# Kernel tuning notes

Measured on AMD Instinct MI355X. Metric: run time of the kernel, lower is better.

Reference implementation:

```python
import jax, jax.numpy as jnp
import numpy as np

B, CIN, COUT, H, W = 8, 128, 256, 64, 64
EPS = 1e-5


def conv2d(x, w, b, pad):
    y = jax.lax.conv_general_dilated(
        x, w, window_strides=(1, 1), padding=[(pad, pad), (pad, pad)],
        dimension_numbers=('NCHW', 'OIHW', 'NCHW'))
    return y + b[None, :, None, None]


def deform_sample(x, offset):
    # x: [B,C,H,W], offset: [B,18,H,W] -> sampled: [B,C,9,H,W]
    b, c, h, w = x.shape
    off = offset.reshape(b, 9, 2, h, w)  # (dy, dx) per kernel tap (torchvision v1 order)
    ky = (jnp.arange(9) // 3 - 1).astype(x.dtype)
    kx = (jnp.arange(9) % 3 - 1).astype(x.dtype)
    py = jnp.arange(h, dtype=x.dtype)[None, None, :, None] + ky[None, :, None, None] + off[:, :, 0]
    px = jnp.arange(w, dtype=x.dtype)[None, None, None, :] + kx[None, :, None, None] + off[:, :, 1]
    y0 = jnp.floor(py); x0 = jnp.floor(px)
    fy = py - y0;       fx = px - x0
    xf = x.reshape(b, c, h * w)

    def gather(iy, ix):
        valid = (iy >= 0) & (iy < h) & (ix >= 0) & (ix < w)
        iyc = jnp.clip(iy, 0, h - 1).astype(jnp.int32)
        ixc = jnp.clip(ix, 0, w - 1).astype(jnp.int32)
        idx = (iyc * w + ixc).reshape(b, -1)  # [B, 9*H*W]
        g = jax.vmap(lambda xb, ib: jnp.take(xb, ib, axis=1))(xf, idx)  # [B,C,9HW]
        return g.reshape(b, c, 9, h, w) * valid.astype(x.dtype)[:, None]

    samp = (gather(y0,     x0    ) * ((1 - fy) * (1 - fx))[:, None]
          + gather(y0,     x0 + 1) * ((1 - fy) * fx      )[:, None]
          + gather(y0 + 1, x0    ) * (fy * (1 - fx)      )[:, None]
          + gather(y0 + 1, x0 + 1) * (fy * fx            )[:, None])
    return samp


def setup_inputs():
    key = jax.random.key(0)
    ks = jax.random.split(key, 8)
    return {
        'x':     jax.random.normal(ks[0], (B, CIN, H, W), jnp.float32),
        'w_off': jax.random.normal(ks[1], (18, CIN, 3, 3), jnp.float32) * 0.01,
        'b_off': jnp.zeros((18,), jnp.float32),
        'w_def': jax.random.normal(ks[2], (COUT, CIN, 3, 3), jnp.float32) * 0.03,
        'b_def': jax.random.normal(ks[3], (COUT,), jnp.float32) * 0.01,
        'gamma': jnp.ones((COUT,), jnp.float32),
        'beta':  jnp.zeros((COUT,), jnp.float32),
        'w_sc':  jax.random.normal(ks[4], (COUT, CIN, 1, 1), jnp.float32) * 0.05,
        'b_sc':  jnp.zeros((COUT,), jnp.float32),
    }


def reference(x, w_off, b_off, w_def, b_def, gamma, beta, w_sc, b_sc):
    offset = conv2d(x, w_off, b_off, pad=1)                 # [B,18,H,W]
    samp = deform_sample(x, offset)                         # [B,C,9,H,W]
    out = jnp.einsum('bckhw,ock->bohw', samp, w_def.reshape(COUT, CIN, 9))
    out = out + b_def[None, :, None, None]
    # BatchNorm2d (training mode: batch statistics)
    mean = out.mean(axis=(0, 2, 3))
    var = out.var(axis=(0, 2, 3))
    out = (out - mean[None, :, None, None]) * jax.lax.rsqrt(var + EPS)[None, :, None, None]
    out = out * gamma[None, :, None, None] + beta[None, :, None, None]
    out = out + conv2d(x, w_sc, b_sc, pad=0)                # residual shortcut (1x1)
    return jax.nn.relu(out)
```

## Files before the change

### kernel.cpp

```cpp
#include <hip/hip_runtime.h>

typedef __attribute__((ext_vector_type(8))) short bf16x8;
typedef __attribute__((ext_vector_type(4))) float f32x4;

__device__ __forceinline__ float bf2f(unsigned short u) {
  return __uint_as_float(((unsigned int)u) << 16);
}
__device__ __forceinline__ unsigned short f2bf(float f) {
  unsigned int u = __float_as_uint(f);
  u += 0x7fffu + ((u >> 16) & 1u);
  return (unsigned short)(u >> 16);
}

constexpr size_t OFF_XPAD = 0;
constexpr size_t SZ_XPAD  = (size_t)8 * 66 * 66 * 128 * 2;
constexpr size_t OFF_WB   = OFF_XPAD + SZ_XPAD;
constexpr size_t SZ_WB    = (size_t)9 * 16 * 256 * 8 * 2;
constexpr size_t OFF_WS2  = OFF_WB + SZ_WB;
constexpr size_t SZ_WS2   = (size_t)16 * 256 * 8 * 2;
constexpr size_t OFF_WO   = OFF_WS2 + SZ_WS2;
constexpr size_t SZ_WO    = (size_t)9 * 16 * 32 * 8 * 2;
constexpr size_t OFF_YM   = OFF_WO + SZ_WO;
constexpr size_t SZ_YM    = (size_t)32768 * 256 * 2;
constexpr size_t OFF_PART = OFF_YM + SZ_YM;
constexpr size_t SZ_PART  = (size_t)1024 * 256 * 2 * 4;
constexpr size_t OFF_STAT = OFF_PART + SZ_PART;

__global__ __launch_bounds__(256) void k_prep_x(const float* __restrict__ x,
                                                unsigned short* __restrict__ xp) {
  int blk = blockIdx.x;
  int b = blk >> 6, h = blk & 63;
  int t = threadIdx.x;
  __shared__ float tile[16][66];

  {
    unsigned short* base = xp + (size_t)b * 66 * 66 * 128;
    ushort4 z4 = {0, 0, 0, 0};
    if (t < 64) {
      int col = (t >> 5) ? 65 : 0;
      int i = t & 31;
      *(ushort4*)(base + ((size_t)(h + 1) * 66 + col) * 128 + i * 4) = z4;
    }
    if (h == 0) {
      for (int i = t; i < 2112; i += 256) {
        *(ushort4*)(base + (size_t)i * 4) = z4;
        *(ushort4*)(base + (size_t)65 * 66 * 128 + (size_t)i * 4) = z4;
      }
    }
  }

  for (int cc = 0; cc < 8; ++cc) {
    int c0 = cc * 16;
    int wr = t & 63, cl = t >> 6;
#pragma unroll
    for (int i = 0; i < 4; ++i) {
      int c = c0 + cl * 4 + i;
      tile[cl * 4 + i][wr] = x[(((size_t)b * 128 + c) * 64 + h) * 64 + wr];
    }
    __syncthreads();
    int ww = t >> 2, cq = t & 3;
    ushort4 u4;
    u4.x = f2bf(tile[cq * 4 + 0][ww]);
    u4.y = f2bf(tile[cq * 4 + 1][ww]);
    u4.z = f2bf(tile[cq * 4 + 2][ww]);
    u4.w = f2bf(tile[cq * 4 + 3][ww]);
    *(ushort4*)(xp + ((size_t)(b * 66 + h + 1) * 66 + (ww + 1)) * 128 + c0 + cq * 4) = u4;
    __syncthreads();
  }
}

__global__ __launch_bounds__(256) void k_pack_w(const float* __restrict__ wdef,
                                                const float* __restrict__ wsc,
                                                const float* __restrict__ woff,
                                                unsigned short* __restrict__ wB,
                                                unsigned short* __restrict__ wS,
                                                unsigned short* __restrict__ wO) {
  int tid = blockIdx.x * 256 + threadIdx.x;
  if (tid < 294912) {
    int k8 = tid & 7, n = (tid >> 3) & 255, kb = (tid >> 11) & 15, tap = tid >> 15;
    int c = kb * 8 + k8;
    wB[tid] = f2bf(wdef[((size_t)n * 128 + c) * 9 + tap]);
  } else if (tid < 294912 + 32768) {
    int i = tid - 294912;
    int k8 = i & 7, n = (i >> 3) & 255, kb = i >> 11;
    wS[i] = f2bf(wsc[(size_t)n * 128 + kb * 8 + k8]);
  } else if (tid < 294912 + 32768 + 36864) {
    int i = tid - 327680;
    int k8 = i & 7, n = (i >> 3) & 31, kb = (i >> 8) & 15, tap = i >> 12;
    int c = kb * 8 + k8;
    wO[i] = f2bf(n < 18 ? woff[((size_t)n * 128 + c) * 9 + tap] : 0.f);
  }
}

__global__ __launch_bounds__(256) void k_main(const unsigned short* __restrict__ xp,
                                              const unsigned short* __restrict__ wB,
                                              const unsigned short* __restrict__ wO,
                                              const float* __restrict__ boff,
                                              const float* __restrict__ bdef,
                                              unsigned short* __restrict__ ymain,
                                              float* __restrict__ partials) {
  int blk = blockIdx.x;
  int b = blk >> 7, rem = blk & 127, h = rem >> 1, half = rem & 1;
  int px0 = half * 32;
  int t = threadIdx.x;
  int lane = t & 63, wid = t >> 6;
  int m = lane & 15, quad = lane >> 4;
  __shared__ __align__(16) unsigned short At[2][32 * 136];
  __shared__ float offsL[9][32][2];

  if (wid < 2) {
    f32x4 a0 = {0.f, 0.f, 0.f, 0.f}, a1 = {0.f, 0.f, 0.f, 0.f};
    int px = px0 + wid * 16 + m;
    const unsigned short* xbase = xp + ((size_t)(b * 66 + h) * 66 + px) * 128 + quad * 8;
    for (int tap = 0; tap < 9; ++tap) {
      const unsigned short* arow = xbase + ((tap / 3) * 66 + (tap % 3)) * 128;
#pragma unroll
      for (int kk = 0; kk < 4; ++kk) {
        bf16x8 a = *(const bf16x8*)(arow + kk * 32);
        const unsigned short* bb = wO + (size_t)(tap * 16 + kk * 4 + quad) * 256;
        bf16x8 b0 = *(const bf16x8*)(bb + m * 8);
        bf16x8 b1 = *(const bf16x8*)(bb + (16 + m) * 8);
        a0 = __builtin_amdgcn_mfma_f32_16x16x32_bf16(a, b0, a0, 0, 0, 0);
        a1 = __builtin_amdgcn_mfma_f32_16x16x32_bf16(a, b1, a1, 0, 0, 0);
      }
    }
#pragma unroll
    for (int r = 0; r < 4; ++r) {
      int pxs = wid * 16 + quad * 4 + r;
      offsL[m >> 1][pxs][m & 1] = a0[r] + boff[m];
      if (m < 2) offsL[8][pxs][m] = a1[r] + boff[16 + m];
    }
  }
  __syncthreads();

  f32x4 acc[2][4];
#pragma unroll
  for (int i = 0; i < 2; ++i)
#pragma unroll
    for (int j = 0; j < 4; ++j) acc[i][j] = (f32x4){0.f, 0.f, 0.f, 0.f};

  int px_s = t >> 3, sub = t & 7;
  const unsigned short* xb_base = xp + (size_t)b * 66 * 66 * 128;
  int nb = wid * 64;

  auto sample_prep = [&](int tap, float* wgt, const unsigned short** p) {
    float2 ov = *(const float2*)&offsL[tap][px_s][0];
    int ky = tap / 3 - 1, kx = tap % 3 - 1;
    float py = (float)(h + ky) + ov.x;
    float pxf = (float)(px0 + px_s + kx) + ov.y;
    float y0f = floorf(py), x0f = floorf(pxf);
    float fy = py - y0f, fx = pxf - x0f;
    int iy0 = (int)y0f, ix0 = (int)x0f;
#pragma unroll
    for (int j = 0; j < 4; ++j) {
      int iy = iy0 + (j >> 1), ix = ix0 + (j & 1);
      float wy = (j >> 1) ? fy : 1.f - fy;
      float wx = (j & 1) ? fx : 1.f - fx;
      bool valid = (iy >= 0) && (iy < 64) && (ix >= 0) && (ix < 64);
      int iyc = min(max(iy, 0), 63), ixc = min(max(ix, 0), 63);
      wgt[j] = valid ? wy * wx : 0.f;
      p[j] = xb_base + ((size_t)(iyc + 1) * 66 + (ixc + 1)) * 128 + sub * 8;
    }
  };
  auto load_g1 = [&](const unsigned short** p, int g, bf16x8* v) {
#pragma unroll
    for (int j = 0; j < 4; ++j)
      v[j] = *(const bf16x8*)(p[j] + g * 64);
  };
  auto store_g1 = [&](unsigned short* dst, int g, const float* wgt, bf16x8* v) {
    bf16x8 o;
#pragma unroll
    for (int j = 0; j < 8; ++j) {
      float s = fmaf(wgt[0], bf2f((unsigned short)v[0][j]),
                fmaf(wgt[1], bf2f((unsigned short)v[1][j]),
                fmaf(wgt[2], bf2f((unsigned short)v[2][j]),
                     wgt[3] * bf2f((unsigned short)v[3][j]))));
      o[j] = (short)f2bf(s);
    }
    *(bf16x8*)(dst + g * 64) = o;
  };
  auto mfma_half = [&](const unsigned short* buf, int tap, int kk0) {
#pragma unroll
    for (int kk = kk0; kk < kk0 + 2; ++kk) {
      bf16x8 af[2];
#pragma unroll
      for (int ms = 0; ms < 2; ++ms)
        af[ms] = *(const bf16x8*)(buf + (ms * 16 + m) * 136 + kk * 32 + quad * 8);
#pragma unroll
      for (int ns = 0; ns < 4; ++ns) {
        bf16x8 bfr = *(const bf16x8*)(wB + ((size_t)(tap * 16 + kk * 4 + quad) * 256 + nb + ns * 16 + m) * 8);
#pragma unroll
        for (int ms = 0; ms < 2; ++ms)
          acc[ms][ns] = __builtin_amdgcn_mfma_f32_16x16x32_bf16(af[ms], bfr, acc[ms][ns], 0, 0, 0);
      }
    }
  };

  {
    float wgt[4]; const unsigned short* p[4]; bf16x8 v0[4], v1[4];
    sample_prep(0, wgt, p);
    unsigned short* dst = &At[0][px_s * 136 + sub * 8];
    load_g1(p, 0, v0); load_g1(p, 1, v1);
    store_g1(dst, 0, wgt, v0); store_g1(dst, 1, wgt, v1);
  }
#pragma unroll
  for (int tap = 0; tap < 9; ++tap) {
    __syncthreads();
    const unsigned short* cur = At[tap & 1];
    unsigned short* dst = &At[(tap + 1) & 1][px_s * 136 + sub * 8];
    if (tap < 8) {
      float wgt[4]; const unsigned short* p[4]; bf16x8 v0[4], v1[4];
      sample_prep(tap + 1, wgt, p);
      load_g1(p, 0, v0);
      load_g1(p, 1, v1);
      mfma_half(cur, tap, 0);
      store_g1(dst, 0, wgt, v0);
      mfma_half(cur, tap, 2);
      store_g1(dst, 1, wgt, v1);
    } else {
      mfma_half(cur, tap, 0);
      mfma_half(cur, tap, 2);
    }
  }

  __syncthreads();
  unsigned short* yb = &At[0][0];
#pragma unroll
  for (int ns = 0; ns < 4; ++ns) {
    int n = nb + ns * 16 + m;
    float bias = bdef[n];
    float s = 0.f, q = 0.f;
#pragma unroll
    for (int ms = 0; ms < 2; ++ms) {
#pragma unroll
      for (int r = 0; r < 4; ++r) {
        int px = ms * 16 + quad * 4 + r;
        float v = acc[ms][ns][r] + bias;
        yb[px * 264 + n] = f2bf(v);
        s += v;
        q += v * v;
      }
    }
    s += __shfl_xor(s, 16); s += __shfl_xor(s, 32);
    q += __shfl_xor(q, 16); q += __shfl_xor(q, 32);
    if (quad == 0) {
      partials[((size_t)blk * 256 + n) * 2 + 0] = s;
      partials[((size_t)blk * 256 + n) * 2 + 1] = q;
    }
  }
  __syncthreads();
  {
    unsigned short* grow = ymain + (size_t)(blk * 32 + px_s) * 256;
    const unsigned short* lrow = yb + px_s * 264;
#pragma unroll
    for (int k = 0; k < 4; ++k) {
      int n0 = k * 64 + sub * 8;
      *(bf16x8*)(grow + n0) = *(const bf16x8*)(lrow + n0);
    }
  }
}

__global__ __launch_bounds__(64) void k_stats(const float* __restrict__ partials,
                                              const float* __restrict__ gamma,
                                              const float* __restrict__ beta,
                                              float* __restrict__ stats) {
  int ch = blockIdx.x;
  int L = threadIdx.x;
  float s = 0.f, q = 0.f;
#pragma unroll
  for (int i = 0; i < 16; ++i) {
    int row = i * 64 + L;
    float2 pq = *(const float2*)&partials[((size_t)row * 256 + ch) * 2];
    s += pq.x;
    q += pq.y;
  }
#pragma unroll
  for (int d = 1; d < 64; d <<= 1) { s += __shfl_xor(s, d); q += __shfl_xor(q, d); }
  if (L == 0) {
    float mean = s * (1.f / 32768.f);
    float var = q * (1.f / 32768.f) - mean * mean;
    float inv = rsqrtf(var + 1e-5f);
    float A = gamma[ch] * inv;
    stats[ch * 2 + 0] = A;
    stats[ch * 2 + 1] = beta[ch] - mean * A;
  }
}

__global__ __launch_bounds__(256) void k_final(const unsigned short* __restrict__ xp,
                                               const unsigned short* __restrict__ wS,
                                               const unsigned short* __restrict__ ymain,
                                               const float* __restrict__ stats,
                                               const float* __restrict__ bsc,
                                               float* __restrict__ out) {
  int blk = blockIdx.x;
  int b = blk >> 7, rem = blk & 127, h = rem >> 1, half = rem & 1;
  int px0 = half * 32;
  int t = threadIdx.x;
  int lane = t & 63, wid = t >> 6;
  int m = lane & 15, quad = lane >> 4;
  __shared__ float tr[128 * 35];
  f32x4 acc[2][4];
#pragma unroll
  for (int i = 0; i < 2; ++i)
#pragma unroll
    for (int j = 0; j < 4; ++j) acc[i][j] = (f32x4){0.f, 0.f, 0.f, 0.f};
  const unsigned short* xrow = xp + ((size_t)(b * 66 + h + 1) * 66 + 1 + px0) * 128;
  int nb = wid * 64;
#pragma unroll
  for (int kk = 0; kk < 4; ++kk) {
    bf16x8 af[2];
#pragma unroll
    for (int ms = 0; ms < 2; ++ms)
      af[ms] = *(const bf16x8*)(xrow + (ms * 16 + m) * 128 + kk * 32 + quad * 8);
#pragma unroll
    for (int ns = 0; ns < 4; ++ns) {
      bf16x8 bfr = *(const bf16x8*)(wS + ((size_t)(kk * 4 + quad) * 256 + nb + ns * 16 + m) * 8);
#pragma unroll
      for (int ms = 0; ms < 2; ++ms)
        acc[ms][ns] = __builtin_amdgcn_mfma_f32_16x16x32_bf16(af[ms], bfr, acc[ms][ns], 0, 0, 0);
    }
  }
  for (int pass = 0; pass < 2; ++pass) {
    if ((wid >> 1) == pass) {
#pragma unroll
      for (int ns = 0; ns < 4; ++ns) {
        int n = nb + ns * 16 + m;
        float bs = bsc[n];
        int nl = n - pass * 128;
#pragma unroll
        for (int ms = 0; ms < 2; ++ms)
#pragma unroll
          for (int r = 0; r < 4; ++r) {
            int px = ms * 16 + quad * 4 + r;
            tr[nl * 35 + px] = acc[ms][ns][r] + bs;
          }
      }
    }
    __syncthreads();
    {
      int nl2 = t & 63, g = t >> 6;
      int n = pass * 128 + nl2 * 2;
      float A0 = stats[n * 2 + 0], B0 = stats[n * 2 + 1];
      float A1 = stats[n * 2 + 2], B1 = stats[n * 2 + 3];
#pragma unroll
      for (int i = 0; i < 8; ++i) {
        int pxl = g * 8 + i;
        unsigned int ym2 = *(const unsigned int*)(ymain + (size_t)(blk * 32 + pxl) * 256 + n);
        float y0 = bf2f((unsigned short)(ym2 & 0xffffu));
        float y1 = bf2f((unsigned short)(ym2 >> 16));
        int nl = nl2 * 2;
        float* p0 = &tr[nl * 35 + pxl];
        float* p1 = &tr[(nl + 1) * 35 + pxl];
        *p0 = fmaxf(fmaf(y0, A0, B0) + *p0, 0.f);
        *p1 = fmaxf(fmaf(y1, A1, B1) + *p1, 0.f);
      }
    }
    __syncthreads();
    {
      int ww = t & 31, ng = t >> 5;
#pragma unroll
      for (int i = 0; i < 16; ++i) {
        int nl = ng * 16 + i;
        out[((size_t)(b * 256 + pass * 128 + nl) * 64 + h) * 64 + px0 + ww] = tr[nl * 35 + ww];
      }
    }
    __syncthreads();
  }
}

extern "C" void kernel_launch(void* const* d_in, const int* in_sizes, int n_in,
                              void* d_out, int out_size, void* d_ws, size_t ws_size,
                              hipStream_t stream) {
  const float* x     = (const float*)d_in[0];
  const float* w_off = (const float*)d_in[1];
  const float* b_off = (const float*)d_in[2];
  const float* w_def = (const float*)d_in[3];
  const float* b_def = (const float*)d_in[4];
  const float* gamma = (const float*)d_in[5];
  const float* beta  = (const float*)d_in[6];
  const float* w_sc  = (const float*)d_in[7];
  const float* b_sc  = (const float*)d_in[8];
  float* out = (float*)d_out;

  char* ws = (char*)d_ws;
  unsigned short* xpad  = (unsigned short*)(ws + OFF_XPAD);
  unsigned short* wB    = (unsigned short*)(ws + OFF_WB);
  unsigned short* wS    = (unsigned short*)(ws + OFF_WS2);
  unsigned short* wO    = (unsigned short*)(ws + OFF_WO);
  unsigned short* ymain = (unsigned short*)(ws + OFF_YM);
  float* partials       = (float*)(ws + OFF_PART);
  float* stats          = (float*)(ws + OFF_STAT);

  k_prep_x<<<512, 256, 0, stream>>>(x, xpad);
  k_pack_w<<<1424, 256, 0, stream>>>(w_def, w_sc, w_off, wB, wS, wO);
  k_main<<<1024, 256, 0, stream>>>(xpad, wB, wO, b_off, b_def, ymain, partials);
  k_stats<<<256, 64, 0, stream>>>(partials, gamma, beta, stats);
  k_final<<<1024, 256, 0, stream>>>(xpad, wS, ymain, stats, b_sc, out);
}
```

Measured before the change: 169.7 us.

## Process full 64-pixel rows per block in deformable conv main kernel

k_main now handles a whole image row (64 pixels) per block instead of half a row. That doubles the M tile to 4 MFMA subtiles per wave, so each weight fragment loaded from global memory is reused twice as often, and the number of blocks and partial-stat rows is halved. Block indices are remapped so batch is the fastest-varying dimension in all kernels, which changes L2 locality, and ymain stores become nontemporal. The cost is more accumulator registers and LDS per block, which can lower occupancy, plus only 512 blocks to spread across the CUs.

```diff
diff --git a/kernel.cpp b/kernel.cpp
--- a/kernel.cpp
+++ b/kernel.cpp
@@ -23,13 +23,14 @@
 constexpr size_t OFF_YM   = OFF_WO + SZ_WO;
 constexpr size_t SZ_YM    = (size_t)32768 * 256 * 2;
 constexpr size_t OFF_PART = OFF_YM + SZ_YM;
-constexpr size_t SZ_PART  = (size_t)1024 * 256 * 2 * 4;
+constexpr size_t SZ_PART  = (size_t)512 * 256 * 2 * 4;
 constexpr size_t OFF_STAT = OFF_PART + SZ_PART;
+
 
 __global__ __launch_bounds__(256) void k_prep_x(const float* __restrict__ x,
                                                 unsigned short* __restrict__ xp) {
   int blk = blockIdx.x;
-  int b = blk >> 6, h = blk & 63;
+  int b = blk & 7, h = blk >> 3;
   int t = threadIdx.x;
   __shared__ float tile[16][66];
 
@@ -100,17 +101,17 @@
                                               unsigned short* __restrict__ ymain,
                                               float* __restrict__ partials) {
   int blk = blockIdx.x;
-  int b = blk >> 7, rem = blk & 127, h = rem >> 1, half = rem & 1;
-  int px0 = half * 32;
+  int b = blk & 7, h = blk >> 3;
+  int bh = (b << 6) + h;
   int t = threadIdx.x;
   int lane = t & 63, wid = t >> 6;
   int m = lane & 15, quad = lane >> 4;
-  __shared__ __align__(16) unsigned short At[2][32 * 136];
-  __shared__ float offsL[9][32][2];
-
-  if (wid < 2) {
+  __shared__ __align__(16) unsigned short At[2][64 * 136];
+  __shared__ float offsL[9][64][2];
+
+  {
     f32x4 a0 = {0.f, 0.f, 0.f, 0.f}, a1 = {0.f, 0.f, 0.f, 0.f};
-    int px = px0 + wid * 16 + m;
+    int px = wid * 16 + m;
     const unsigned short* xbase = xp + ((size_t)(b * 66 + h) * 66 + px) * 128 + quad * 8;
     for (int tap = 0; tap < 9; ++tap) {
       const unsigned short* arow = xbase + ((tap / 3) * 66 + (tap % 3)) * 128;
@@ -133,13 +134,13 @@
   }
   __syncthreads();
 
-  f32x4 acc[2][4];
-#pragma unroll
-  for (int i = 0; i < 2; ++i)
+  f32x4 acc[4][4];
+#pragma unroll
+  for (int i = 0; i < 4; ++i)
 #pragma unroll
     for (int j = 0; j < 4; ++j) acc[i][j] = (f32x4){0.f, 0.f, 0.f, 0.f};
 
-  int px_s = t >> 3, sub = t & 7;
+  int px_s = t >> 2, sub = t & 3;
   const unsigned short* xb_base = xp + (size_t)b * 66 * 66 * 128;
   int nb = wid * 64;
 
@@ -147,7 +148,7 @@
     float2 ov = *(const float2*)&offsL[tap][px_s][0];
     int ky = tap / 3 - 1, kx = tap % 3 - 1;
     float py = (float)(h + ky) + ov.x;
-    float pxf = (float)(px0 + px_s + kx) + ov.y;
+    float pxf = (float)(px_s + kx) + ov.y;
     float y0f = floorf(py), x0f = floorf(pxf);
     float fy = py - y0f, fx = pxf - x0f;
     int iy0 = (int)y0f, ix0 = (int)x0f;
@@ -162,46 +163,51 @@
       p[j] = xb_base + ((size_t)(iyc + 1) * 66 + (ixc + 1)) * 128 + sub * 8;
     }
   };
-  auto load_g1 = [&](const unsigned short** p, int g, bf16x8* v) {
-#pragma unroll
-    for (int j = 0; j < 4; ++j)
-      v[j] = *(const bf16x8*)(p[j] + g * 64);
+  auto load_g2 = [&](const unsigned short** p, int g0, bf16x8 (*v)[4]) {
+#pragma unroll
+    for (int gg = 0; gg < 2; ++gg)
+#pragma unroll
+      for (int j = 0; j < 4; ++j)
+        v[gg][j] = *(const bf16x8*)(p[j] + (g0 + gg) * 32);
   };
-  auto store_g1 = [&](unsigned short* dst, int g, const float* wgt, bf16x8* v) {
-    bf16x8 o;
-#pragma unroll
-    for (int j = 0; j < 8; ++j) {
-      float s = fmaf(wgt[0], bf2f((unsigned short)v[0][j]),
-                fmaf(wgt[1], bf2f((unsigned short)v[1][j]),
-                fmaf(wgt[2], bf2f((unsigned short)v[2][j]),
-                     wgt[3] * bf2f((unsigned short)v[3][j]))));
-      o[j] = (short)f2bf(s);
-    }
-    *(bf16x8*)(dst + g * 64) = o;
+  auto store_g2 = [&](unsigned short* dst, int g0, const float* wgt, bf16x8 (*v)[4]) {
+#pragma unroll
+    for (int gg = 0; gg < 2; ++gg) {
+      bf16x8 o;
+#pragma unroll
+      for (int j = 0; j < 8; ++j) {
+        float s = fmaf(wgt[0], bf2f((unsigned short)v[gg][0][j]),
+                  fmaf(wgt[1], bf2f((unsigned short)v[gg][1][j]),
+                  fmaf(wgt[2], bf2f((unsigned short)v[gg][2][j]),
+                       wgt[3] * bf2f((unsigned short)v[gg][3][j]))));
+        o[j] = (short)f2bf(s);
+      }
+      *(bf16x8*)(dst + (g0 + gg) * 32) = o;
+    }
   };
   auto mfma_half = [&](const unsigned short* buf, int tap, int kk0) {
 #pragma unroll
     for (int kk = kk0; kk < kk0 + 2; ++kk) {
-      bf16x8 af[2];
-#pragma unroll
-      for (int ms = 0; ms < 2; ++ms)
+      bf16x8 af[4];
+#pragma unroll
+      for (int ms = 0; ms < 4; ++ms)
         af[ms] = *(const bf16x8*)(buf + (ms * 16 + m) * 136 + kk * 32 + quad * 8);
 #pragma unroll
       for (int ns = 0; ns < 4; ++ns) {
         bf16x8 bfr = *(const bf16x8*)(wB + ((size_t)(tap * 16 + kk * 4 + quad) * 256 + nb + ns * 16 + m) * 8);
 #pragma unroll
-        for (int ms = 0; ms < 2; ++ms)
+        for (int ms = 0; ms < 4; ++ms)
           acc[ms][ns] = __builtin_amdgcn_mfma_f32_16x16x32_bf16(af[ms], bfr, acc[ms][ns], 0, 0, 0);
       }
     }
   };
 
   {
-    float wgt[4]; const unsigned short* p[4]; bf16x8 v0[4], v1[4];
+    float wgt[4]; const unsigned short* p[4]; bf16x8 v[2][4];
     sample_prep(0, wgt, p);
     unsigned short* dst = &At[0][px_s * 136 + sub * 8];
-    load_g1(p, 0, v0); load_g1(p, 1, v1);
-    store_g1(dst, 0, wgt, v0); store_g1(dst, 1, wgt, v1);
+    load_g2(p, 0, v); store_g2(dst, 0, wgt, v);
+    load_g2(p, 2, v); store_g2(dst, 2, wgt, v);
   }
 #pragma unroll
   for (int tap = 0; tap < 9; ++tap) {
@@ -209,14 +215,14 @@
     const unsigned short* cur = At[tap & 1];
     unsigned short* dst = &At[(tap + 1) & 1][px_s * 136 + sub * 8];
     if (tap < 8) {
-      float wgt[4]; const unsigned short* p[4]; bf16x8 v0[4], v1[4];
+      float wgt[4]; const unsigned short* p[4]; bf16x8 v[2][4];
       sample_prep(tap + 1, wgt, p);
-      load_g1(p, 0, v0);
-      load_g1(p, 1, v1);
+      load_g2(p, 0, v);
       mfma_half(cur, tap, 0);
-      store_g1(dst, 0, wgt, v0);
+      store_g2(dst, 0, wgt, v);
+      load_g2(p, 2, v);
       mfma_half(cur, tap, 2);
-      store_g1(dst, 1, wgt, v1);
+      store_g2(dst, 2, wgt, v);
     } else {
       mfma_half(cur, tap, 0);
       mfma_half(cur, tap, 2);
@@ -231,7 +237,7 @@
     float bias = bdef[n];
     float s = 0.f, q = 0.f;
 #pragma unroll
-    for (int ms = 0; ms < 2; ++ms) {
+    for (int ms = 0; ms < 4; ++ms) {
 #pragma unroll
       for (int r = 0; r < 4; ++r) {
         int px = ms * 16 + quad * 4 + r;
@@ -250,12 +256,12 @@
   }
   __syncthreads();
   {
-    unsigned short* grow = ymain + (size_t)(blk * 32 + px_s) * 256;
+    unsigned short* grow = ymain + (size_t)(bh * 64 + px_s) * 256;
     const unsigned short* lrow = yb + px_s * 264;
 #pragma unroll
-    for (int k = 0; k < 4; ++k) {
-      int n0 = k * 64 + sub * 8;
-      *(bf16x8*)(grow + n0) = *(const bf16x8*)(lrow + n0);
+    for (int k = 0; k < 8; ++k) {
+      int n0 = k * 32 + sub * 8;
+      __builtin_nontemporal_store(*(const bf16x8*)(lrow + n0), (bf16x8*)(grow + n0));
     }
   }
 }
@@ -268,7 +274,7 @@
   int L = threadIdx.x;
   float s = 0.f, q = 0.f;
 #pragma unroll
-  for (int i = 0; i < 16; ++i) {
+  for (int i = 0; i < 8; ++i) {
     int row = i * 64 + L;
     float2 pq = *(const float2*)&partials[((size_t)row * 256 + ch) * 2];
     s += pq.x;
@@ -293,8 +299,9 @@
                                                const float* __restrict__ bsc,
                                                float* __restrict__ out) {
   int blk = blockIdx.x;
-  int b = blk >> 7, rem = blk & 127, h = rem >> 1, half = rem & 1;
+  int b = blk & 7, rem = blk >> 3, h = rem >> 1, half = rem & 1;
   int px0 = half * 32;
+  int bh = (b << 6) + h;
   int t = threadIdx.x;
   int lane = t & 63, wid = t >> 6;
   int m = lane & 15, quad = lane >> 4;
@@ -345,7 +352,7 @@
 #pragma unroll
       for (int i = 0; i < 8; ++i) {
         int pxl = g * 8 + i;
-        unsigned int ym2 = *(const unsigned int*)(ymain + (size_t)(blk * 32 + pxl) * 256 + n);
+        unsigned int ym2 = *(const unsigned int*)(ymain + (size_t)(bh * 64 + px0 + pxl) * 256 + n);
         float y0 = bf2f((unsigned short)(ym2 & 0xffffu));
         float y1 = bf2f((unsigned short)(ym2 >> 16));
         int nl = nl2 * 2;
@@ -393,7 +400,7 @@
 
   k_prep_x<<<512, 256, 0, stream>>>(x, xpad);
   k_pack_w<<<1424, 256, 0, stream>>>(w_def, w_sc, w_off, wB, wS, wO);
-  k_main<<<1024, 256, 0, stream>>>(xpad, wB, wO, b_off, b_def, ymain, partials);
+  k_main<<<512, 256, 0, stream>>>(xpad, wB, wO, b_off, b_def, ymain, partials);
   k_stats<<<256, 64, 0, stream>>>(partials, gamma, beta, stats);
   k_final<<<1024, 256, 0, stream>>>(xpad, wS, ymain, stats, b_sc, out);
 }
```

Result: faster. 160.3 us (-5.5%).

## Widen main tile to full row with 512 threads, merge prep kernels

Applied to the files above, without the earlier changes.

The main kernel now processes a full 64-pixel row per block with 512 threads (8 waves, 32 output channels each) instead of half-rows with 256 threads. Each weight fragment is reused across four M-subtiles, and the offset conv covers the whole row in one pass. The x-prep and weight-pack kernels are merged into one launch, block order is interleaved by batch, and ymain stores become nontemporal. LDS use per block doubles, which may limit occupancy.

```diff
diff --git a/kernel.cpp b/kernel.cpp
--- a/kernel.cpp
+++ b/kernel.cpp
@@ -23,16 +23,40 @@
 constexpr size_t OFF_YM   = OFF_WO + SZ_WO;
 constexpr size_t SZ_YM    = (size_t)32768 * 256 * 2;
 constexpr size_t OFF_PART = OFF_YM + SZ_YM;
-constexpr size_t SZ_PART  = (size_t)1024 * 256 * 2 * 4;
+constexpr size_t SZ_PART  = (size_t)512 * 256 * 2 * 4;
 constexpr size_t OFF_STAT = OFF_PART + SZ_PART;
 
-__global__ __launch_bounds__(256) void k_prep_x(const float* __restrict__ x,
-                                                unsigned short* __restrict__ xp) {
+
+__global__ __launch_bounds__(256) void k_prep(const float* __restrict__ x,
+                                              unsigned short* __restrict__ xp,
+                                              const float* __restrict__ wdef,
+                                              const float* __restrict__ wsc,
+                                              const float* __restrict__ woff,
+                                              unsigned short* __restrict__ wB,
+                                              unsigned short* __restrict__ wS,
+                                              unsigned short* __restrict__ wO) {
+  int t = threadIdx.x;
+  if (blockIdx.x >= 512) {
+    int tid = (blockIdx.x - 512) * 256 + t;
+    if (tid < 294912) {
+      int k8 = tid & 7, n = (tid >> 3) & 255, kb = (tid >> 11) & 15, tap = tid >> 15;
+      int c = kb * 8 + k8;
+      wB[tid] = f2bf(wdef[((size_t)n * 128 + c) * 9 + tap]);
+    } else if (tid < 294912 + 32768) {
+      int i = tid - 294912;
+      int k8 = i & 7, n = (i >> 3) & 255, kb = i >> 11;
+      wS[i] = f2bf(wsc[(size_t)n * 128 + kb * 8 + k8]);
+    } else if (tid < 294912 + 32768 + 36864) {
+      int i = tid - 327680;
+      int k8 = i & 7, n = (i >> 3) & 31, kb = (i >> 8) & 15, tap = i >> 12;
+      int c = kb * 8 + k8;
+      wO[i] = f2bf(n < 18 ? woff[((size_t)n * 128 + c) * 9 + tap] : 0.f);
+    }
+    return;
+  }
   int blk = blockIdx.x;
-  int b = blk >> 6, h = blk & 63;
-  int t = threadIdx.x;
+  int b = blk & 7, h = blk >> 3;
   __shared__ float tile[16][66];
-
   {
     unsigned short* base = xp + (size_t)b * 66 * 66 * 128;
     ushort4 z4 = {0, 0, 0, 0};
@@ -48,7 +72,6 @@
       }
     }
   }
-
   for (int cc = 0; cc < 8; ++cc) {
     int c0 = cc * 16;
     int wr = t & 63, cl = t >> 6;
@@ -69,48 +92,25 @@
   }
 }
 
-__global__ __launch_bounds__(256) void k_pack_w(const float* __restrict__ wdef,
-                                                const float* __restrict__ wsc,
-                                                const float* __restrict__ woff,
-                                                unsigned short* __restrict__ wB,
-                                                unsigned short* __restrict__ wS,
-                                                unsigned short* __restrict__ wO) {
-  int tid = blockIdx.x * 256 + threadIdx.x;
-  if (tid < 294912) {
-    int k8 = tid & 7, n = (tid >> 3) & 255, kb = (tid >> 11) & 15, tap = tid >> 15;
-    int c = kb * 8 + k8;
-    wB[tid] = f2bf(wdef[((size_t)n * 128 + c) * 9 + tap]);
-  } else if (tid < 294912 + 32768) {
-    int i = tid - 294912;
-    int k8 = i & 7, n = (i >> 3) & 255, kb = i >> 11;
-    wS[i] = f2bf(wsc[(size_t)n * 128 + kb * 8 + k8]);
-  } else if (tid < 294912 + 32768 + 36864) {
-    int i = tid - 327680;
-    int k8 = i & 7, n = (i >> 3) & 31, kb = (i >> 8) & 15, tap = i >> 12;
-    int c = kb * 8 + k8;
-    wO[i] = f2bf(n < 18 ? woff[((size_t)n * 128 + c) * 9 + tap] : 0.f);
-  }
-}
-
-__global__ __launch_bounds__(256) void k_main(const unsigned short* __restrict__ xp,
-                                              const unsigned short* __restrict__ wB,
-                                              const unsigned short* __restrict__ wO,
-                                              const float* __restrict__ boff,
-                                              const float* __restrict__ bdef,
-                                              unsigned short* __restrict__ ymain,
-                                              float* __restrict__ partials) {
+__global__ __launch_bounds__(512, 4) void k_main(const unsigned short* __restrict__ xp,
+                                                 const unsigned short* __restrict__ wB,
+                                                 const unsigned short* __restrict__ wO,
+                                                 const float* __restrict__ boff,
+                                                 const float* __restrict__ bdef,
+                                                 unsigned short* __restrict__ ymain,
+                                                 float* __restrict__ partials) {
   int blk = blockIdx.x;
-  int b = blk >> 7, rem = blk & 127, h = rem >> 1, half = rem & 1;
-  int px0 = half * 32;
+  int b = blk & 7, h = blk >> 3;
+  int bh = (b << 6) + h;
   int t = threadIdx.x;
   int lane = t & 63, wid = t >> 6;
   int m = lane & 15, quad = lane >> 4;
-  __shared__ __align__(16) unsigned short At[2][32 * 136];
-  __shared__ float offsL[9][32][2];
-
-  if (wid < 2) {
+  __shared__ __align__(16) unsigned short At[2][64 * 136];
+  __shared__ float offsL[9][64][2];
+
+  if (wid < 4) {
     f32x4 a0 = {0.f, 0.f, 0.f, 0.f}, a1 = {0.f, 0.f, 0.f, 0.f};
-    int px = px0 + wid * 16 + m;
+    int px = wid * 16 + m;
     const unsigned short* xbase = xp + ((size_t)(b * 66 + h) * 66 + px) * 128 + quad * 8;
     for (int tap = 0; tap < 9; ++tap) {
       const unsigned short* arow = xbase + ((tap / 3) * 66 + (tap % 3)) * 128;
@@ -133,21 +133,21 @@
   }
   __syncthreads();
 
-  f32x4 acc[2][4];
-#pragma unroll
-  for (int i = 0; i < 2; ++i)
-#pragma unroll
-    for (int j = 0; j < 4; ++j) acc[i][j] = (f32x4){0.f, 0.f, 0.f, 0.f};
+  f32x4 acc[4][2];
+#pragma unroll
+  for (int i = 0; i < 4; ++i)
+#pragma unroll
+    for (int j = 0; j < 2; ++j) acc[i][j] = (f32x4){0.f, 0.f, 0.f, 0.f};
 
   int px_s = t >> 3, sub = t & 7;
   const unsigned short* xb_base = xp + (size_t)b * 66 * 66 * 128;
-  int nb = wid * 64;
+  int nb = wid * 32;
 
   auto sample_prep = [&](int tap, float* wgt, const unsigned short** p) {
     float2 ov = *(const float2*)&offsL[tap][px_s][0];
     int ky = tap / 3 - 1, kx = tap % 3 - 1;
     float py = (float)(h + ky) + ov.x;
-    float pxf = (float)(px0 + px_s + kx) + ov.y;
+    float pxf = (float)(px_s + kx) + ov.y;
     float y0f = floorf(py), x0f = floorf(pxf);
     float fy = py - y0f, fx = pxf - x0f;
     int iy0 = (int)y0f, ix0 = (int)x0f;
@@ -182,15 +182,15 @@
   auto mfma_half = [&](const unsigned short* buf, int tap, int kk0) {
 #pragma unroll
     for (int kk = kk0; kk < kk0 + 2; ++kk) {
-      bf16x8 af[2];
-#pragma unroll
-      for (int ms = 0; ms < 2; ++ms)
+      bf16x8 af[4];
+#pragma unroll
+      for (int ms = 0; ms < 4; ++ms)
         af[ms] = *(const bf16x8*)(buf + (ms * 16 + m) * 136 + kk * 32 + quad * 8);
 #pragma unroll
-      for (int ns = 0; ns < 4; ++ns) {
+      for (int ns = 0; ns < 2; ++ns) {
         bf16x8 bfr = *(const bf16x8*)(wB + ((size_t)(tap * 16 + kk * 4 + quad) * 256 + nb + ns * 16 + m) * 8);
 #pragma unroll
-        for (int ms = 0; ms < 2; ++ms)
+        for (int ms = 0; ms < 4; ++ms)
           acc[ms][ns] = __builtin_amdgcn_mfma_f32_16x16x32_bf16(af[ms], bfr, acc[ms][ns], 0, 0, 0);
       }
     }
@@ -226,12 +226,12 @@
   __syncthreads();
   unsigned short* yb = &At[0][0];
 #pragma unroll
-  for (int ns = 0; ns < 4; ++ns) {
+  for (int ns = 0; ns < 2; ++ns) {
     int n = nb + ns * 16 + m;
     float bias = bdef[n];
     float s = 0.f, q = 0.f;
 #pragma unroll
-    for (int ms = 0; ms < 2; ++ms) {
+    for (int ms = 0; ms < 4; ++ms) {
 #pragma unroll
       for (int r = 0; r < 4; ++r) {
         int px = ms * 16 + quad * 4 + r;
@@ -250,12 +250,12 @@
   }
   __syncthreads();
   {
-    unsigned short* grow = ymain + (size_t)(blk * 32 + px_s) * 256;
+    unsigned short* grow = ymain + (size_t)(bh * 64 + px_s) * 256;
     const unsigned short* lrow = yb + px_s * 264;
 #pragma unroll
     for (int k = 0; k < 4; ++k) {
       int n0 = k * 64 + sub * 8;
-      *(bf16x8*)(grow + n0) = *(const bf16x8*)(lrow + n0);
+      __builtin_nontemporal_store(*(const bf16x8*)(lrow + n0), (bf16x8*)(grow + n0));
     }
   }
 }
@@ -268,7 +268,7 @@
   int L = threadIdx.x;
   float s = 0.f, q = 0.f;
 #pragma unroll
-  for (int i = 0; i < 16; ++i) {
+  for (int i = 0; i < 8; ++i) {
     int row = i * 64 + L;
     float2 pq = *(const float2*)&partials[((size_t)row * 256 + ch) * 2];
     s += pq.x;
@@ -293,8 +293,9 @@
                                                const float* __restrict__ bsc,
                                                float* __restrict__ out) {
   int blk = blockIdx.x;
-  int b = blk >> 7, rem = blk & 127, h = rem >> 1, half = rem & 1;
+  int b = blk & 7, rem = blk >> 3, h = rem >> 1, half = rem & 1;
   int px0 = half * 32;
+  int bh = (b << 6) + h;
   int t = threadIdx.x;
   int lane = t & 63, wid = t >> 6;
   int m = lane & 15, quad = lane >> 4;
@@ -345,7 +346,7 @@
 #pragma unroll
       for (int i = 0; i < 8; ++i) {
         int pxl = g * 8 + i;
-        unsigned int ym2 = *(const unsigned int*)(ymain + (size_t)(blk * 32 + pxl) * 256 + n);
+        unsigned int ym2 = *(const unsigned int*)(ymain + (size_t)(bh * 64 + px0 + pxl) * 256 + n);
         float y0 = bf2f((unsigned short)(ym2 & 0xffffu));
         float y1 = bf2f((unsigned short)(ym2 >> 16));
         int nl = nl2 * 2;
@@ -391,9 +392,8 @@
   float* partials       = (float*)(ws + OFF_PART);
   float* stats          = (float*)(ws + OFF_STAT);
 
-  k_prep_x<<<512, 256, 0, stream>>>(x, xpad);
-  k_pack_w<<<1424, 256, 0, stream>>>(w_def, w_sc, w_off, wB, wS, wO);
-  k_main<<<1024, 256, 0, stream>>>(xpad, wB, wO, b_off, b_def, ymain, partials);
+  k_prep<<<1936, 256, 0, stream>>>(x, xpad, w_def, w_sc, w_off, wB, wS, wO);
+  k_main<<<512, 512, 0, stream>>>(xpad, wB, wO, b_off, b_def, ymain, partials);
   k_stats<<<256, 64, 0, stream>>>(partials, gamma, beta, stats);
   k_final<<<1024, 256, 0, stream>>>(xpad, wS, ymain, stats, b_sc, out);
 }
```

Result: faster. 152.7 us (-10.0%).
